# Performance work log

Measured on AMD Instinct MI355X. Metric: run time of the kernel, lower is better.

## Reference

```python
import jax, jax.numpy as jnp
import numpy as np

M = 4096  # rows (axis -2), cosine transform axis
N = 4096  # cols (axis -1), sine transform axis


def setup_inputs() -> dict:
    key = jax.random.key(0)
    x = jax.random.normal(key, (M, N), dtype=jnp.float32)
    return {"x": x}


def _cos_basis(n):
    # C[u, p] = cos(pi * (2u+1) * p / (2n))  -- IDXCT basis (no coefficient normalization)
    u = jnp.arange(n, dtype=jnp.float32)
    p = jnp.arange(n, dtype=jnp.float32)
    return jnp.cos(jnp.pi * (2.0 * u[:, None] + 1.0) * p[None, :] / (2.0 * n))


def _sin_basis(n):
    # S[v, q] = sin(pi * (2v+1) * q / (2n))  -- IDXST basis (q=0 column is zero)
    v = jnp.arange(n, dtype=jnp.float32)
    q = jnp.arange(n, dtype=jnp.float32)
    return jnp.sin(jnp.pi * (2.0 * v[:, None] + 1.0) * q[None, :] / (2.0 * n))


def reference(x):
    # idcst2(x) = idxct(idxst(x)^T)^T
    # y_{u,v} = sum_p sum_q x_{p,q} * cos(pi*p*(2u+1)/(2M)) * sin(pi*q*(2v+1)/(2N))
    m, n = x.shape[-2], x.shape[-1]
    C0 = _cos_basis(m).astype(x.dtype)  # [M, M]
    S1 = _sin_basis(n).astype(x.dtype)  # [N, N]
    y = jnp.matmul(x, S1.T)   # IDXST along last axis: [M, N]
    out = jnp.matmul(C0, y)   # IDXCT along axis -2:  [M, N]
    return out
```

## Files before the change

### kernel.cpp

```cpp
#include <hip/hip_runtime.h>


#define NF 4096
#define TWOPI_16384 3.8349519697141029e-4f
#define TWOPI_4096  1.5339807878856412e-3f
#define TWOPI_256   2.4543692606170259e-2f

__device__ __forceinline__ float2 cmul(float2 a, float2 b) {
    return make_float2(a.x * b.x - a.y * b.y, a.x * b.y + a.y * b.x);
}
__device__ __forceinline__ float2 cadd(float2 a, float2 b) {
    return make_float2(a.x + b.x, a.y + b.y);
}
__device__ __forceinline__ float2 csub(float2 a, float2 b) {
    return make_float2(a.x - b.x, a.y - b.y);
}
__device__ __forceinline__ float2 muli(float2 a) {
    return make_float2(-a.y, a.x);
}

__device__ __forceinline__ void fft16(float2 f[16]) {
    float2 s[16];
#pragma unroll
    for (int b = 0; b < 4; ++b) {
        float2 x0 = f[b], x1 = f[b + 4], x2 = f[b + 8], x3 = f[b + 12];
        float2 t0 = cadd(x0, x2), t1 = csub(x0, x2);
        float2 t2 = cadd(x1, x3), t3 = csub(x1, x3);
        s[b]      = cadd(t0, t2);
        s[4 + b]  = cadd(t1, muli(t3));
        s[8 + b]  = csub(t0, t2);
        s[12 + b] = csub(t1, muli(t3));
    }
    const float2 w1 = make_float2(0.92387953251128674f, 0.38268343236508977f);
    const float2 w2 = make_float2(0.70710678118654752f, 0.70710678118654752f);
    const float2 w3 = make_float2(0.38268343236508977f, 0.92387953251128674f);
    const float2 w6 = make_float2(-0.70710678118654752f, 0.70710678118654752f);
    const float2 w9 = make_float2(-0.92387953251128674f, -0.38268343236508977f);
    s[5]  = cmul(s[5], w1);
    s[6]  = cmul(s[6], w2);
    s[7]  = cmul(s[7], w3);
    s[9]  = cmul(s[9], w2);
    s[10] = muli(s[10]);
    s[11] = cmul(s[11], w6);
    s[13] = cmul(s[13], w3);
    s[14] = cmul(s[14], w6);
    s[15] = cmul(s[15], w9);
#pragma unroll
    for (int al = 0; al < 4; ++al) {
        float2 x0 = s[4 * al + 0], x1 = s[4 * al + 1];
        float2 x2 = s[4 * al + 2], x3 = s[4 * al + 3];
        float2 t0 = cadd(x0, x2), t1 = csub(x0, x2);
        float2 t2 = cadd(x1, x3), t3 = csub(x1, x3);
        f[al]      = cadd(t0, t2);
        f[4 + al]  = cadd(t1, muli(t3));
        f[8 + al]  = csub(t0, t2);
        f[12 + al] = csub(t1, muli(t3));
    }
}

__device__ __forceinline__ void fftA_store(float2 r[16], float2* __restrict__ buf,
                                           const int t) {
    fft16(r);
    float sn, cs;
    __sincosf((float)t * TWOPI_4096, &sn, &cs);
    const float2 wb = make_float2(cs, sn);
    float2 w = wb;
#pragma unroll
    for (int k1 = 1; k1 < 16; ++k1) { r[k1] = cmul(r[k1], w); w = cmul(w, wb); }
#pragma unroll
    for (int i = 0; i < 16; ++i) buf[i * 256 + t] = r[i];
}

__device__ __forceinline__ void fft4096_tail(float2* __restrict__ buf, const int t) {
    float2 r[16];
    __syncthreads();
    {
        const int k1 = t >> 4, m2 = t & 15;
        const int base = k1 * 256 + m2;
#pragma unroll
        for (int i = 0; i < 16; ++i) r[i] = buf[base + i * 16];
        fft16(r);
        float sn, cs;
        __sincosf((float)m2 * TWOPI_256, &sn, &cs);
        const float2 wb = make_float2(cs, sn);
        float2 w = wb;
#pragma unroll
        for (int j1 = 1; j1 < 16; ++j1) { r[j1] = cmul(r[j1], w); w = cmul(w, wb); }
        const int bw = k1 * 256 + (m2 ^ k1);
#pragma unroll
        for (int j1 = 0; j1 < 16; ++j1) buf[bw + j1 * 16] = r[j1];
    }
    __syncthreads();
    {
        const int k1 = t & 15;
        const int bc = k1 * 256 + (t >> 4) * 16;
#pragma unroll
        for (int i = 0; i < 16; ++i) r[i] = buf[bc + (i ^ k1)];
        fft16(r);
        __syncthreads();
#pragma unroll
        for (int j2 = 0; j2 < 16; ++j2) buf[j2 * 256 + t] = r[j2];
    }
    __syncthreads();
}

__global__ __launch_bounds__(256) void dst_rows_k(const float* __restrict__ x,
                                                  float* __restrict__ y) {
    __shared__ float2 buf[4096];
    const int t = threadIdx.x;
    const size_t r0 = (size_t)blockIdx.x * 2;
    const float* x0 = x + r0 * NF;
    const float* x1 = x0 + NF;

    float sn, cs;
    __sincosf((float)t * TWOPI_16384, &sn, &cs);
    float2 w = make_float2(0.5f * cs, 0.5f * sn);
    const float2 stp = make_float2(0.99518472667219693f, 0.09801714032956060f);
    float2 r[16];
#pragma unroll
    for (int i = 0; i < 16; ++i) {
        const int k = t + 256 * i;
        float2 ww = make_float2(0.f, 0.f);
        if (k > 0) {
            float re = x0[NF - k] + x1[k];
            float im = x1[NF - k] - x0[k];
            ww = make_float2(re * w.x - im * w.y, re * w.y + im * w.x);
        }
        r[i] = ww;
        w = cmul(w, stp);
    }
    fftA_store(r, buf, t);
    fft4096_tail(buf, t);

    float* y0 = y + r0 * NF;
    float* y1 = y0 + NF;
#pragma unroll
    for (int u = 0; u < 8; ++u) {
        const int n = t + 256 * u;
        float2 vn = buf[n];
        float2 vm = buf[NF - 1 - n];
        ((float2*)y0)[n] = make_float2(vn.x, -vm.x);
        ((float2*)y1)[n] = make_float2(vn.y, -vm.y);
    }
}

__global__ __launch_bounds__(256) void colpass1_k(const float* __restrict__ y,
                                                  float2* __restrict__ H) {
    const int tid = threadIdx.x;
    const int cl = tid & 31;
    const int sl = tid >> 5;
    const int bs = blockIdx.x & 15;
    const int bc = blockIdx.x >> 4;
    const int cpg = bc * 32 + cl;
    const int c0 = 2 * cpg;
    const float2 stp = make_float2(0.99518472667219693f, 0.09801714032956060f);

#pragma unroll
    for (int ii = 0; ii < 2; ++ii) {
        const int s = 16 * bs + ii * 8 + sl;
        float2 f[16];
        float sn, cs;
        __sincosf((float)s * TWOPI_16384, &sn, &cs);
        float2 w = make_float2(0.5f * cs, 0.5f * sn);
#pragma unroll
        for (int j = 0; j < 16; ++j) {
            const int k = j * 256 + s;
            if (k == 0) {
                float2 r0v = *(const float2*)(y + c0);
                f[j] = make_float2(0.5f * r0v.x, 0.5f * r0v.y);
            } else {
                float2 A = *(const float2*)(y + (size_t)k * NF + c0);
                float2 Bm = *(const float2*)(y + (size_t)(NF - k) * NF + c0);
                float re = A.x + Bm.y;
                float im = A.y - Bm.x;
                f[j] = make_float2(re * w.x - im * w.y, re * w.y + im * w.x);
            }
            w = cmul(w, stp);
        }
        fft16(f);
        __sincosf((float)s * TWOPI_4096, &sn, &cs);
        const float2 wb = make_float2(cs, sn);
        float2 wa = wb;
#pragma unroll
        for (int a = 1; a < 16; ++a) { f[a] = cmul(f[a], wa); wa = cmul(wa, wb); }
#pragma unroll
        for (int a = 0; a < 16; ++a)
            H[(size_t)(a * 256 + s) * 2048 + cpg] = f[a];
    }
}

__global__ __launch_bounds__(256) void colpass2_k(const float2* __restrict__ H,
                                                  const float* __restrict__ y,
                                                  float* __restrict__ out) {
    __shared__ float2 lds[8192];
    const int tid = threadIdx.x;
    const int cp = tid & 15;
    const int g = tid >> 4;
    const int ap = blockIdx.x & 7;
    const int bc = blockIdx.x >> 3;
    const int cpg = bc * 16 + cp;
    const int c0 = 2 * cpg;
    int aabs0 = ap, aabs1 = 15 - ap;

#pragma unroll
    for (int A = 0; A < 2; ++A) {
        const int abase = (A ? aabs1 : aabs0) * 256;
        float2 f[16];
#pragma unroll
        for (int s1 = 0; s1 < 16; ++s1)
            f[s1] = H[(size_t)(abase + 16 * s1 + g) * 2048 + cpg];
        fft16(f);
        float sn, cs;
        __sincosf((float)g * TWOPI_256, &sn, &cs);
        const float2 wb = make_float2(cs, sn);
        float2 w = wb;
#pragma unroll
        for (int b = 1; b < 16; ++b) { f[b] = cmul(f[b], w); w = cmul(w, wb); }
#pragma unroll
        for (int b = 0; b < 16; ++b)
            lds[((A * 16 + b) * 16 + g) * 16 + cp] = f[b];
    }
    __syncthreads();

    float2 v0[16], v1[16];
    {
        float2 f[16];
#pragma unroll
        for (int s0 = 0; s0 < 16; ++s0) f[s0] = lds[(g * 16 + s0) * 16 + cp];
        fft16(f);
#pragma unroll
        for (int c = 0; c < 16; ++c) v0[c] = f[c];
#pragma unroll
        for (int s0 = 0; s0 < 16; ++s0)
            f[s0] = lds[((16 + g) * 16 + s0) * 16 + cp];
        fft16(f);
#pragma unroll
        for (int c = 0; c < 16; ++c) v1[c] = f[c];
    }
    __syncthreads();

#pragma unroll
    for (int c = 0; c < 16; ++c) {
        lds[(g + 16 * c) * 16 + cp] = v0[c];
        lds[(256 + g + 16 * c) * 16 + cp] = v1[c];
    }
    __syncthreads();

    float2 h0 = *(const float2*)(y + c0);
    const float a0h = 0.5f * h0.x, a1h = 0.5f * h0.y;
    const int aout = g >> 3;
    const int mh = g & 7;
    const int na = aout ? aabs1 : aabs0;
#pragma unroll
    for (int mi = 0; mi < 16; ++mi) {
        const int m = mh * 16 + mi;
        const int n = na + 16 * m;
        float2 vA = lds[(aout * 256 + m) * 16 + cp];
        float2 vB = lds[((1 - aout) * 256 + (255 - m)) * 16 + cp];
        *(float2*)(out + (size_t)(2 * n) * NF + c0) =
            make_float2(vA.x + a0h, vA.y + a1h);
        *(float2*)(out + (size_t)(2 * n + 1) * NF + c0) =
            make_float2(vB.x + a0h, vB.y + a1h);
    }
}

__global__ __launch_bounds__(256) void dct_rows_k(const float* __restrict__ yt,
                                                  float* __restrict__ ot) {
    __shared__ float2 buf[4096];
    const int t = threadIdx.x;
    const size_t r0 = (size_t)blockIdx.x * 2;
    const float* t0 = yt + r0 * NF;
    const float* t1 = t0 + NF;
    const float a0h = 0.5f * t0[0];
    const float a1h = 0.5f * t1[0];

    float sn, cs;
    __sincosf((float)t * TWOPI_16384, &sn, &cs);
    float2 w = make_float2(0.5f * cs, 0.5f * sn);
    const float2 stp = make_float2(0.99518472667219693f, 0.09801714032956060f);
    float2 r[16];
#pragma unroll
    for (int i = 0; i < 16; ++i) {
        const int k = t + 256 * i;
        if (k == 0) {
            r[i] = make_float2(a0h, a1h);
        } else {
            float re = t0[k] + t1[NF - k];
            float im = t1[k] - t0[NF - k];
            r[i] = make_float2(re * w.x - im * w.y, re * w.y + im * w.x);
        }
        w = cmul(w, stp);
    }
    fftA_store(r, buf, t);
    fft4096_tail(buf, t);

    float* o0 = ot + r0 * NF;
    float* o1 = o0 + NF;
#pragma unroll
    for (int u = 0; u < 8; ++u) {
        const int n = t + 256 * u;
        float2 vn = buf[n];
        float2 vm = buf[NF - 1 - n];
        ((float2*)o0)[n] = make_float2(vn.x + a0h, vm.x + a0h);
        ((float2*)o1)[n] = make_float2(vn.y + a1h, vm.y + a1h);
    }
}

__global__ __launch_bounds__(256) void transpose_k(const float* __restrict__ in,
                                                   float* __restrict__ out) {
    __shared__ float tile[32][33];
    const int tx = threadIdx.x;
    const int ty = threadIdx.y;
    const int c0 = blockIdx.x * 32;
    const int r0 = blockIdx.y * 32;

    float4 v = *(const float4*)(in + (size_t)(r0 + ty) * NF + c0 + 4 * tx);
    tile[ty][4 * tx + 0] = v.x;
    tile[ty][4 * tx + 1] = v.y;
    tile[ty][4 * tx + 2] = v.z;
    tile[ty][4 * tx + 3] = v.w;
    __syncthreads();

    float4 o;
    o.x = tile[4 * tx + 0][ty];
    o.y = tile[4 * tx + 1][ty];
    o.z = tile[4 * tx + 2][ty];
    o.w = tile[4 * tx + 3][ty];
    *(float4*)(out + (size_t)(c0 + ty) * NF + r0 + 4 * tx) = o;
}

extern "C" void kernel_launch(void* const* d_in, const int* in_sizes, int n_in,
                              void* d_out, int out_size, void* d_ws, size_t ws_size,
                              hipStream_t stream) {
    const float* x = (const float*)d_in[0];
    float* out = (float*)d_out;
    float* y = (float*)d_ws;

    if (ws_size >= ((size_t)128 << 20)) {
        float2* H = (float2*)(y + ((size_t)64 << 20) / 4);
        dst_rows_k<<<2048, 256, 0, stream>>>(x, y);
        colpass1_k<<<1024, 256, 0, stream>>>(y, H);
        colpass2_k<<<1024, 256, 0, stream>>>(H, y, out);
    } else {
        dim3 tgrid(128, 128), tblk(8, 32);
        dst_rows_k<<<2048, 256, 0, stream>>>(x, y);
        transpose_k<<<tgrid, tblk, 0, stream>>>(y, out);
        dct_rows_k<<<2048, 256, 0, stream>>>(out, y);
        transpose_k<<<tgrid, tblk, 0, stream>>>(y, out);
    }
}
```

Measured before the change: 179.7 us.

## Halve per-block work in column FFT passes and double grid size

colpass1 now handles one s-slice per thread instead of two, and its grid is doubled. colpass2 now processes a single 'a' group per block instead of a mirrored pair. Each output is written directly from registers, with the mirrored rows computed from an index formula, which removes the LDS transpose round trip and two barriers. This halves LDS use and register arrays to raise occupancy and parallelism. The cost is more blocks and less coalesced output rows for the mirrored half.

```diff
diff --git a/kernel.cpp b/kernel.cpp
--- a/kernel.cpp
+++ b/kernel.cpp
@@ -149,66 +149,60 @@
     const int tid = threadIdx.x;
     const int cl = tid & 31;
     const int sl = tid >> 5;
-    const int bs = blockIdx.x & 15;
-    const int bc = blockIdx.x >> 4;
+    const int bs = blockIdx.x & 31;
+    const int bc = blockIdx.x >> 5;
     const int cpg = bc * 32 + cl;
     const int c0 = 2 * cpg;
+    const int s = 8 * bs + sl;
     const float2 stp = make_float2(0.99518472667219693f, 0.09801714032956060f);
 
-#pragma unroll
-    for (int ii = 0; ii < 2; ++ii) {
-        const int s = 16 * bs + ii * 8 + sl;
-        float2 f[16];
-        float sn, cs;
-        __sincosf((float)s * TWOPI_16384, &sn, &cs);
-        float2 w = make_float2(0.5f * cs, 0.5f * sn);
-#pragma unroll
-        for (int j = 0; j < 16; ++j) {
-            const int k = j * 256 + s;
-            if (k == 0) {
-                float2 r0v = *(const float2*)(y + c0);
-                f[j] = make_float2(0.5f * r0v.x, 0.5f * r0v.y);
-            } else {
-                float2 A = *(const float2*)(y + (size_t)k * NF + c0);
-                float2 Bm = *(const float2*)(y + (size_t)(NF - k) * NF + c0);
-                float re = A.x + Bm.y;
-                float im = A.y - Bm.x;
-                f[j] = make_float2(re * w.x - im * w.y, re * w.y + im * w.x);
-            }
-            w = cmul(w, stp);
+    float2 f[16];
+    float sn, cs;
+    __sincosf((float)s * TWOPI_16384, &sn, &cs);
+    float2 w = make_float2(0.5f * cs, 0.5f * sn);
+#pragma unroll
+    for (int j = 0; j < 16; ++j) {
+        const int k = j * 256 + s;
+        if (k == 0) {
+            float2 r0v = *(const float2*)(y + c0);
+            f[j] = make_float2(0.5f * r0v.x, 0.5f * r0v.y);
+        } else {
+            float2 A = *(const float2*)(y + (size_t)k * NF + c0);
+            float2 Bm = *(const float2*)(y + (size_t)(NF - k) * NF + c0);
+            float re = A.x + Bm.y;
+            float im = A.y - Bm.x;
+            f[j] = make_float2(re * w.x - im * w.y, re * w.y + im * w.x);
         }
-        fft16(f);
-        __sincosf((float)s * TWOPI_4096, &sn, &cs);
-        const float2 wb = make_float2(cs, sn);
-        float2 wa = wb;
-#pragma unroll
-        for (int a = 1; a < 16; ++a) { f[a] = cmul(f[a], wa); wa = cmul(wa, wb); }
-#pragma unroll
-        for (int a = 0; a < 16; ++a)
-            H[(size_t)(a * 256 + s) * 2048 + cpg] = f[a];
-    }
+        w = cmul(w, stp);
+    }
+    fft16(f);
+    __sincosf((float)s * TWOPI_4096, &sn, &cs);
+    const float2 wb = make_float2(cs, sn);
+    float2 wa = wb;
+#pragma unroll
+    for (int a = 1; a < 16; ++a) { f[a] = cmul(f[a], wa); wa = cmul(wa, wb); }
+#pragma unroll
+    for (int a = 0; a < 16; ++a)
+        H[(size_t)(a * 256 + s) * 2048 + cpg] = f[a];
 }
 
 __global__ __launch_bounds__(256) void colpass2_k(const float2* __restrict__ H,
                                                   const float* __restrict__ y,
                                                   float* __restrict__ out) {
-    __shared__ float2 lds[8192];
+    __shared__ float2 lds[4096];
     const int tid = threadIdx.x;
     const int cp = tid & 15;
     const int g = tid >> 4;
-    const int ap = blockIdx.x & 7;
-    const int bc = blockIdx.x >> 3;
+    const int a = blockIdx.x & 15;
+    const int bc = blockIdx.x >> 4;
     const int cpg = bc * 16 + cp;
     const int c0 = 2 * cpg;
-    int aabs0 = ap, aabs1 = 15 - ap;
-
-#pragma unroll
-    for (int A = 0; A < 2; ++A) {
-        const int abase = (A ? aabs1 : aabs0) * 256;
+
+    {
         float2 f[16];
 #pragma unroll
         for (int s1 = 0; s1 < 16; ++s1)
-            f[s1] = H[(size_t)(abase + 16 * s1 + g) * 2048 + cpg];
+            f[s1] = H[(size_t)(a * 256 + 16 * s1 + g) * 2048 + cpg];
         fft16(f);
         float sn, cs;
         __sincosf((float)g * TWOPI_256, &sn, &cs);
@@ -218,49 +212,30 @@
         for (int b = 1; b < 16; ++b) { f[b] = cmul(f[b], w); w = cmul(w, wb); }
 #pragma unroll
         for (int b = 0; b < 16; ++b)
-            lds[((A * 16 + b) * 16 + g) * 16 + cp] = f[b];
-    }
-    __syncthreads();
-
-    float2 v0[16], v1[16];
-    {
-        float2 f[16];
-#pragma unroll
-        for (int s0 = 0; s0 < 16; ++s0) f[s0] = lds[(g * 16 + s0) * 16 + cp];
-        fft16(f);
-#pragma unroll
-        for (int c = 0; c < 16; ++c) v0[c] = f[c];
-#pragma unroll
-        for (int s0 = 0; s0 < 16; ++s0)
-            f[s0] = lds[((16 + g) * 16 + s0) * 16 + cp];
-        fft16(f);
-#pragma unroll
-        for (int c = 0; c < 16; ++c) v1[c] = f[c];
-    }
-    __syncthreads();
-
-#pragma unroll
-    for (int c = 0; c < 16; ++c) {
-        lds[(g + 16 * c) * 16 + cp] = v0[c];
-        lds[(256 + g + 16 * c) * 16 + cp] = v1[c];
-    }
-    __syncthreads();
+            lds[(b * 16 + g) * 16 + cp] = f[b];
+    }
+    __syncthreads();
+
+    float2 f[16];
+#pragma unroll
+    for (int s0 = 0; s0 < 16; ++s0) f[s0] = lds[(g * 16 + s0) * 16 + cp];
+    fft16(f);
 
     float2 h0 = *(const float2*)(y + c0);
     const float a0h = 0.5f * h0.x, a1h = 0.5f * h0.y;
-    const int aout = g >> 3;
-    const int mh = g & 7;
-    const int na = aout ? aabs1 : aabs0;
-#pragma unroll
-    for (int mi = 0; mi < 16; ++mi) {
-        const int m = mh * 16 + mi;
-        const int n = na + 16 * m;
-        float2 vA = lds[(aout * 256 + m) * 16 + cp];
-        float2 vB = lds[((1 - aout) * 256 + (255 - m)) * 16 + cp];
+    const int base_n = a + 16 * g;
+#pragma unroll
+    for (int c = 0; c < 8; ++c) {
+        const int n = base_n + 256 * c;
         *(float2*)(out + (size_t)(2 * n) * NF + c0) =
-            make_float2(vA.x + a0h, vA.y + a1h);
-        *(float2*)(out + (size_t)(2 * n + 1) * NF + c0) =
-            make_float2(vB.x + a0h, vB.y + a1h);
+            make_float2(f[c].x + a0h, f[c].y + a1h);
+    }
+#pragma unroll
+    for (int c = 8; c < 16; ++c) {
+        const int n = base_n + 256 * c;
+        const int row = 2 * (4095 - n) + 1;
+        *(float2*)(out + (size_t)row * NF + c0) =
+            make_float2(f[c].x + a0h, f[c].y + a1h);
     }
 }
 
@@ -339,8 +314,8 @@
     if (ws_size >= ((size_t)128 << 20)) {
         float2* H = (float2*)(y + ((size_t)64 << 20) / 4);
         dst_rows_k<<<2048, 256, 0, stream>>>(x, y);
-        colpass1_k<<<1024, 256, 0, stream>>>(y, H);
-        colpass2_k<<<1024, 256, 0, stream>>>(H, y, out);
+        colpass1_k<<<2048, 256, 0, stream>>>(y, H);
+        colpass2_k<<<2048, 256, 0, stream>>>(H, y, out);
     } else {
         dim3 tgrid(128, 128), tblk(8, 32);
         dst_rows_k<<<2048, 256, 0, stream>>>(x, y);
```

Result: slower. 183.9 us (+2.3%).
